# Kernel tuning notes

Hardware: AMD Instinct MI355X
Metric: run time of the kernel (lower is better)

## Reference

```python
import jax, jax.numpy as jnp
import numpy as np

# Config values (from c.mean_shift / c.cuda in the original module)
EMBED_DIM = 32      # embedding_dim
BW = 2.0            # kernel_bandwidth
ETA = 0.5           # step_size
N_ITERS = 3         # nb_iterations
RES = 96            # pic_res (image is RES x RES, N = RES*RES pixels)


def setup_inputs() -> dict:
    key = jax.random.key(0)
    # Scale 0.1 keeps exp(BW * x^T x) well inside fp32 range, mimicking the
    # bounded embeddings produced by the upstream margin-loss-trained net.
    x_in = 0.1 * jax.random.normal(key, (1, EMBED_DIM, RES, RES), dtype=jnp.float32)
    return {"x_in": x_in}


def reference(x_in):
    # x_in: (1, D, RES, RES). One mean-shift step per iteration:
    #   K = exp(bw * X^T X)                      (N x N affinity)
    #   deg_j = sum_i K[i, j]                    (column degree; K is symmetric)
    #   X_new = eta * X @ (K / deg) + (1-eta) * X
    # (The original's torch.inverse(diag(deg)) is exactly 1/deg column scaling.)
    # All iterates are concatenated along dim 0, as in the torch code.
    res = x_in.shape[3]
    n = res * res
    xs = [x_in.reshape(EMBED_DIM, n)]
    for _ in range(N_ITERS):
        X = xs[-1]                                    # (D, N)
        K = jnp.exp(BW * jnp.einsum('di,dj->ij', X, X))  # (N, N)
        deg = K.sum(axis=0)                           # (N,) column sums
        xs.append(ETA * (X @ (K / deg)) + (1.0 - ETA) * X)
    # (N_ITERS+1, D, RES, RES)
    return jnp.stack(xs, axis=0).reshape(-1, EMBED_DIM, res, res)
```

## Files before the change

kernel.cpp:

```cpp
#include <hip/hip_runtime.h>
#include <hip/hip_bf16.h>


#define DIM 32
#define RESO 96
#define NPT (RESO * RESO)
#define NITER 3
#define ETA 0.5f
#define SCALE 2.88539008f

#define QB 128
#define NQB (NPT / QB)
#define KSEG 7
#define NCHUNK128 (NPT / 128)

typedef __bf16 bf16_t;
typedef __bf16 v8bf __attribute__((ext_vector_type(8)));
typedef float  v4f  __attribute__((ext_vector_type(4)));

__device__ __forceinline__ void gload_lds16(const bf16_t* g, bf16_t* l) {
    __builtin_amdgcn_global_load_lds(
        (const __attribute__((address_space(1))) void*)g,
        (__attribute__((address_space(3))) void*)l, 16, 0, 0);
}

__device__ __forceinline__ int keyinv(int m) {
    return ((m & 8) << 1) | ((m & 4) << 1) | ((m & 16) >> 2) | (m & 3);
}

__global__ __launch_bounds__(256, 4)
void pack_kernel(const float* __restrict__ X,
                 bf16_t* __restrict__ rows,
                 bf16_t* __restrict__ cols,
                 float* __restrict__ out_copy) {
    __shared__ float tt[32][33];
    const int tid = threadIdx.x;
    const int n0  = blockIdx.x * 32;
    const int inv = keyinv(tid & 31);

#pragma unroll
    for (int j = 0; j < 4; ++j) {
        int d = (tid >> 5) + j * 8;
        int n = tid & 31;
        float v = X[(size_t)d * NPT + n0 + n];
        tt[d][n] = v;
        cols[(size_t)d * NPT + n0 + inv] = (bf16_t)v;
        out_copy[(size_t)d * NPT + n0 + n] = v;
    }
    __syncthreads();

#pragma unroll
    for (int j = 0; j < 4; ++j) {
        int n = (tid >> 5) + j * 8;
        int d = tid & 31;
        rows[(size_t)(n0 + n) * DIM + d] = (bf16_t)tt[d][n];
    }
}

__global__ __launch_bounds__(512, 4)
void msattn_kernel(const float* __restrict__ Xcur,
                   const bf16_t* __restrict__ rows,
                   const bf16_t* __restrict__ cols,
                   float* __restrict__ part_num,
                   float* __restrict__ part_den) {
    __shared__ __align__(16) bf16_t tiles[2][8192];

    const int tid  = threadIdx.x;
    const int w    = tid >> 6;
    const int lane = tid & 63;
    const int quad = lane >> 4;
    const int l16  = lane & 15;
    const int qb   = blockIdx.x;
    const int ks   = blockIdx.y;
    const int c0   = (NCHUNK128 * ks) / KSEG;
    const int c1   = (NCHUNK128 * (ks + 1)) / KSEG;
    const int q0w  = qb * QB + w * 16;

    v8bf qfrag;
#pragma unroll
    for (int j = 0; j < 8; ++j) {
        float v = Xcur[(quad * 8 + j) * NPT + q0w + l16];
        qfrag[j] = (bf16_t)(v * SCALE);
    }

    v8bf ones;
#pragma unroll
    for (int j = 0; j < 8; ++j) ones[j] = (bf16_t)1.0f;

    const bf16_t* gsrc;
    int gdelta, hdelta, dstoff;
    if (w < 4) {
        gsrc = rows + ((size_t)c0 * 128 + w * 16 + l16) * DIM + quad * 8;
        gdelta = 128 * DIM;
        hdelta = 64 * DIM;
        dstoff = w * 512;
    } else {
        int r = w - 4, hh = r >> 1, g = r & 1;
        gsrc = cols + (size_t)(hh * 16 + l16) * NPT + c0 * 128 + g * 32 + quad * 8;
        gdelta = 128;
        hdelta = 64;
        dstoff = 2048 + (w - 4) * 512;
    }

    v4f acc0 = {0.f, 0.f, 0.f, 0.f};
    v4f acc1 = {0.f, 0.f, 0.f, 0.f};
    v4f dden = {0.f, 0.f, 0.f, 0.f};

    gload_lds16(gsrc,          &tiles[0][dstoff]);
    gload_lds16(gsrc + hdelta, &tiles[0][4096 + dstoff]);
    gsrc += gdelta;
    __syncthreads();

    for (int c = c0; c < c1; ++c) {
        const int cc = c - c0;
        const bf16_t* tb = tiles[cc & 1];

        if (c + 1 < c1) {
            bf16_t* nt = tiles[(cc + 1) & 1];
            gload_lds16(gsrc,          &nt[dstoff]);
            gload_lds16(gsrc + hdelta, &nt[4096 + dstoff]);
            gsrc += gdelta;
        }

#pragma unroll
        for (int h = 0; h < 2; ++h) {
            const bf16_t* th = tb + h * 4096;

            v4f s[4];
#pragma unroll
            for (int t = 0; t < 4; ++t) {
                v8bf ka = *(const v8bf*)&th[t * 512 + lane * 8];
                s[t] = __builtin_amdgcn_mfma_f32_16x16x32_bf16(ka, qfrag,
                           (v4f){0.f, 0.f, 0.f, 0.f}, 0, 0, 0);
            }

            v8bf b00 = *(const v8bf*)&th[2048 + 0 * 512 + lane * 8];
            v8bf b01 = *(const v8bf*)&th[2048 + 1 * 512 + lane * 8];
            v8bf b10 = *(const v8bf*)&th[2048 + 2 * 512 + lane * 8];
            v8bf b11 = *(const v8bf*)&th[2048 + 3 * 512 + lane * 8];

            v8bf pa0, pa1;
#pragma unroll
            for (int t = 0; t < 2; ++t)
#pragma unroll
                for (int r = 0; r < 4; ++r)
                    pa0[t * 4 + r] = (bf16_t)__builtin_amdgcn_exp2f(s[t][r]);
#pragma unroll
            for (int t = 0; t < 2; ++t)
#pragma unroll
                for (int r = 0; r < 4; ++r)
                    pa1[t * 4 + r] = (bf16_t)__builtin_amdgcn_exp2f(s[2 + t][r]);

            acc0 = __builtin_amdgcn_mfma_f32_16x16x32_bf16(pa0, b00, acc0, 0, 0, 0);
            acc1 = __builtin_amdgcn_mfma_f32_16x16x32_bf16(pa0, b10, acc1, 0, 0, 0);
            dden = __builtin_amdgcn_mfma_f32_16x16x32_bf16(pa0, ones, dden, 0, 0, 0);
            acc0 = __builtin_amdgcn_mfma_f32_16x16x32_bf16(pa1, b01, acc0, 0, 0, 0);
            acc1 = __builtin_amdgcn_mfma_f32_16x16x32_bf16(pa1, b11, acc1, 0, 0, 0);
            dden = __builtin_amdgcn_mfma_f32_16x16x32_bf16(pa1, ones, dden, 0, 0, 0);
        }

        __syncthreads();
    }

    float* pn = part_num + (size_t)ks * NPT * DIM;
#pragma unroll
    for (int r = 0; r < 4; ++r) {
        int gq = q0w + quad * 4 + r;
        pn[(size_t)gq * DIM + l16]      = acc0[r];
        pn[(size_t)gq * DIM + 16 + l16] = acc1[r];
    }
    if (l16 == 0) {
#pragma unroll
        for (int r = 0; r < 4; ++r)
            part_den[ks * NPT + q0w + quad * 4 + r] = dden[r];
    }
}

__global__ __launch_bounds__(256, 4)
void reduce_kernel(const float* __restrict__ part_num,
                   const float* __restrict__ part_den,
                   const float* __restrict__ Xcur,
                   float* __restrict__ Xnext,
                   bf16_t* __restrict__ rows_out,
                   bf16_t* __restrict__ cols_out) {
    __shared__ float tnum[32][33];
    __shared__ float txn[32][33];
    __shared__ float tden[32];

    const int tid = threadIdx.x;
    const int q0  = blockIdx.x * 32;
    const int inv = keyinv(tid & 31);

    {
        int qq = tid >> 3, dq = tid & 7;
        v4f s = {0.f, 0.f, 0.f, 0.f};
#pragma unroll
        for (int ss = 0; ss < KSEG; ++ss)
            s += *(const v4f*)&part_num[((size_t)ss * NPT + q0 + qq) * DIM + dq * 4];
#pragma unroll
        for (int k = 0; k < 4; ++k) tnum[qq][dq * 4 + k] = s[k];
    }
    if (tid < 32) {
        float s = 0.f;
#pragma unroll
        for (int ss = 0; ss < KSEG; ++ss)
            s += part_den[ss * NPT + q0 + tid];
        tden[tid] = s;
    }
    __syncthreads();

#pragma unroll
    for (int j = 0; j < 4; ++j) {
        int idx = tid + j * 256;
        int d = idx >> 5, qq = idx & 31;
        float num = tnum[qq][d];
        float dn  = tden[qq];
        float xo  = Xcur[d * NPT + q0 + qq];
        float xn  = ETA * num / dn + (1.0f - ETA) * xo;
        Xnext[d * NPT + q0 + qq] = xn;
        cols_out[(size_t)d * NPT + q0 + inv] = (bf16_t)xn;
        txn[qq][d] = xn;
    }
    __syncthreads();

#pragma unroll
    for (int j = 0; j < 4; ++j) {
        int idx = tid + j * 256;
        int qq = idx >> 5, d = idx & 31;
        rows_out[(size_t)(q0 + qq) * DIM + d] = (bf16_t)txn[qq][d];
    }
}

extern "C" void kernel_launch(void* const* d_in, const int* in_sizes, int n_in,
                              void* d_out, int out_size, void* d_ws, size_t ws_size,
                              hipStream_t stream) {
    const float* x_in = (const float*)d_in[0];
    float* out = (float*)d_out;

    const size_t DN = (size_t)DIM * NPT;
    bf16_t* rows0 = (bf16_t*)d_ws;
    bf16_t* cols0 = rows0 + DN;
    bf16_t* rows1 = cols0 + DN;
    bf16_t* cols1 = rows1 + DN;
    float* part_num = (float*)(cols1 + DN);
    float* part_den = part_num + (size_t)KSEG * NPT * DIM;

    pack_kernel<<<NPT / 32, 256, 0, stream>>>(x_in, rows0, cols0, out);

    for (int it = 0; it < NITER; ++it) {
        const float* Xcur = (it == 0) ? x_in : out + (size_t)it * DN;
        bf16_t* rin  = (it & 1) ? rows1 : rows0;
        bf16_t* cin  = (it & 1) ? cols1 : cols0;
        bf16_t* rout = (it & 1) ? rows0 : rows1;
        bf16_t* cout = (it & 1) ? cols0 : cols1;
        msattn_kernel<<<dim3(NQB, KSEG), 512, 0, stream>>>(Xcur, rin, cin,
                                                           part_num, part_den);
        reduce_kernel<<<NPT / 32, 256, 0, stream>>>(part_num, part_den, Xcur,
                                                    out + (size_t)(it + 1) * DN,
                                                    rout, cout);
    }
}
```

Baseline: 125.5 us.

## Fuse split-K reduction into attention kernel via last-block atomic counter

Removes the separate reduce kernel. Each attention block now bumps a per-query-block atomic counter, and the last of the KSEG segment blocks to finish sums the partial numerators and denominators. That block then writes the next iterate plus its bf16 row and column copies. This cuts one kernel launch per iteration and its launch gap, at the cost of a serialized reduction tail on the last block and extra fences and atomics.

```diff
diff --git a/kernel.cpp b/kernel.cpp
--- a/kernel.cpp
+++ b/kernel.cpp
@@ -32,11 +32,14 @@
 void pack_kernel(const float* __restrict__ X,
                  bf16_t* __restrict__ rows,
                  bf16_t* __restrict__ cols,
-                 float* __restrict__ out_copy) {
+                 float* __restrict__ out_copy,
+                 int* __restrict__ counters) {
     __shared__ float tt[32][33];
     const int tid = threadIdx.x;
     const int n0  = blockIdx.x * 32;
     const int inv = keyinv(tid & 31);
+
+    if (blockIdx.x == 0 && tid < NQB) counters[tid] = 0;
 
 #pragma unroll
     for (int j = 0; j < 4; ++j) {
@@ -62,8 +65,13 @@
                    const bf16_t* __restrict__ rows,
                    const bf16_t* __restrict__ cols,
                    float* __restrict__ part_num,
-                   float* __restrict__ part_den) {
+                   float* __restrict__ part_den,
+                   float* __restrict__ Xnext,
+                   bf16_t* __restrict__ rows_out,
+                   bf16_t* __restrict__ cols_out,
+                   int* __restrict__ counters) {
     __shared__ __align__(16) bf16_t tiles[2][8192];
+    __shared__ int sflag;
 
     const int tid  = threadIdx.x;
     const int w    = tid >> 6;
@@ -174,60 +182,59 @@
         for (int r = 0; r < 4; ++r)
             part_den[ks * NPT + q0w + quad * 4 + r] = dden[r];
     }
-}
-
-__global__ __launch_bounds__(256, 4)
-void reduce_kernel(const float* __restrict__ part_num,
-                   const float* __restrict__ part_den,
-                   const float* __restrict__ Xcur,
-                   float* __restrict__ Xnext,
-                   bf16_t* __restrict__ rows_out,
-                   bf16_t* __restrict__ cols_out) {
-    __shared__ float tnum[32][33];
-    __shared__ float txn[32][33];
-    __shared__ float tden[32];
-
-    const int tid = threadIdx.x;
-    const int q0  = blockIdx.x * 32;
-    const int inv = keyinv(tid & 31);
-
-    {
-        int qq = tid >> 3, dq = tid & 7;
-        v4f s = {0.f, 0.f, 0.f, 0.f};
+
+    __syncthreads();
+    if (tid == 0) {
+        __threadfence();
+        sflag = __hip_atomic_fetch_add(&counters[qb], 1, __ATOMIC_ACQ_REL,
+                                       __HIP_MEMORY_SCOPE_AGENT);
+    }
+    __syncthreads();
+    if (sflag != KSEG - 1) return;
+    __threadfence();
+    if (tid == 0) counters[qb] = 0;
+
+    float* xsc = (float*)&tiles[0][0];
+    float* dsc = xsc + 128 * 33;
+    const int q0 = qb * QB;
+
+    if (tid < 128) {
+        float sd = 0.f;
+#pragma unroll
+        for (int ss = 0; ss < KSEG; ++ss) sd += part_den[ss * NPT + q0 + tid];
+        dsc[tid] = sd;
+    }
+    __syncthreads();
+
+#pragma unroll
+    for (int j = 0; j < 8; ++j) {
+        int e = j * 512 + tid;
+        int q = e >> 5, d = e & 31;
+        float sn = 0.f;
 #pragma unroll
         for (int ss = 0; ss < KSEG; ++ss)
-            s += *(const v4f*)&part_num[((size_t)ss * NPT + q0 + qq) * DIM + dq * 4];
-#pragma unroll
-        for (int k = 0; k < 4; ++k) tnum[qq][dq * 4 + k] = s[k];
-    }
-    if (tid < 32) {
-        float s = 0.f;
-#pragma unroll
-        for (int ss = 0; ss < KSEG; ++ss)
-            s += part_den[ss * NPT + q0 + tid];
-        tden[tid] = s;
-    }
-    __syncthreads();
-
-#pragma unroll
-    for (int j = 0; j < 4; ++j) {
-        int idx = tid + j * 256;
-        int d = idx >> 5, qq = idx & 31;
-        float num = tnum[qq][d];
-        float dn  = tden[qq];
-        float xo  = Xcur[d * NPT + q0 + qq];
-        float xn  = ETA * num / dn + (1.0f - ETA) * xo;
-        Xnext[d * NPT + q0 + qq] = xn;
-        cols_out[(size_t)d * NPT + q0 + inv] = (bf16_t)xn;
-        txn[qq][d] = xn;
-    }
-    __syncthreads();
-
-#pragma unroll
-    for (int j = 0; j < 4; ++j) {
-        int idx = tid + j * 256;
-        int qq = idx >> 5, d = idx & 31;
-        rows_out[(size_t)(q0 + qq) * DIM + d] = (bf16_t)txn[qq][d];
+            sn += part_num[((size_t)ss * NPT + q0 + q) * DIM + d];
+        xsc[q * 33 + d] = sn;
+    }
+    __syncthreads();
+
+#pragma unroll
+    for (int j = 0; j < 8; ++j) {
+        int e = j * 512 + tid;
+        int d = e >> 7, q = e & 127;
+        float xn = ETA * xsc[q * 33 + d] / dsc[q]
+                 + (1.0f - ETA) * Xcur[(size_t)d * NPT + q0 + q];
+        Xnext[(size_t)d * NPT + q0 + q] = xn;
+        cols_out[(size_t)d * NPT + q0 + (q & ~31) + keyinv(q & 31)] = (bf16_t)xn;
+        xsc[q * 33 + d] = xn;
+    }
+    __syncthreads();
+
+#pragma unroll
+    for (int j = 0; j < 8; ++j) {
+        int e = j * 512 + tid;
+        int q = e >> 5, d = e & 31;
+        rows_out[(size_t)(q0 + q) * DIM + d] = (bf16_t)xsc[q * 33 + d];
     }
 }
 
@@ -244,8 +251,9 @@
     bf16_t* cols1 = rows1 + DN;
     float* part_num = (float*)(cols1 + DN);
     float* part_den = part_num + (size_t)KSEG * NPT * DIM;
-
-    pack_kernel<<<NPT / 32, 256, 0, stream>>>(x_in, rows0, cols0, out);
+    int* counters   = (int*)(part_den + (size_t)KSEG * NPT);
+
+    pack_kernel<<<NPT / 32, 256, 0, stream>>>(x_in, rows0, cols0, out, counters);
 
     for (int it = 0; it < NITER; ++it) {
         const float* Xcur = (it == 0) ? x_in : out + (size_t)it * DN;
@@ -253,10 +261,8 @@
         bf16_t* cin  = (it & 1) ? cols1 : cols0;
         bf16_t* rout = (it & 1) ? rows0 : rows1;
         bf16_t* cout = (it & 1) ? cols0 : cols1;
-        msattn_kernel<<<dim3(NQB, KSEG), 512, 0, stream>>>(Xcur, rin, cin,
-                                                           part_num, part_den);
-        reduce_kernel<<<NPT / 32, 256, 0, stream>>>(part_num, part_den, Xcur,
-                                                    out + (size_t)(it + 1) * DN,
-                                                    rout, cout);
-    }
-}
+        msattn_kernel<<<dim3(NQB, KSEG), 512, 0, stream>>>(
+            Xcur, rin, cin, part_num, part_den,
+            out + (size_t)(it + 1) * DN, rout, cout, counters);
+    }
+}
```

New measurement: 221.0 us. +76.0%, slower.

## Process two query groups per wave to reuse loaded key tiles

Applied to the files above, without the earlier changes.

Each block now handles 256 queries instead of 128, and each wave keeps two query fragments and two sets of accumulators. Every key/value tile staged in LDS is therefore used for twice as many queries, halving global-to-LDS traffic and LDS reads per unit of work. The cost is higher register pressure (launch bounds lowered to 2 blocks per SM) and half as many blocks in the grid (36x7), which reduces the parallelism available across the device.

```diff
diff --git a/kernel.cpp b/kernel.cpp
--- a/kernel.cpp
+++ b/kernel.cpp
@@ -9,7 +9,7 @@
 #define ETA 0.5f
 #define SCALE 2.88539008f
 
-#define QB 128
+#define QB 256
 #define NQB (NPT / QB)
 #define KSEG 7
 #define NCHUNK128 (NPT / 128)
@@ -57,7 +57,7 @@
     }
 }
 
-__global__ __launch_bounds__(512, 4)
+__global__ __launch_bounds__(512, 2)
 void msattn_kernel(const float* __restrict__ Xcur,
                    const bf16_t* __restrict__ rows,
                    const bf16_t* __restrict__ cols,
@@ -76,11 +76,13 @@
     const int c1   = (NCHUNK128 * (ks + 1)) / KSEG;
     const int q0w  = qb * QB + w * 16;
 
-    v8bf qfrag;
+    v8bf qfrag0, qfrag1;
 #pragma unroll
     for (int j = 0; j < 8; ++j) {
-        float v = Xcur[(quad * 8 + j) * NPT + q0w + l16];
-        qfrag[j] = (bf16_t)(v * SCALE);
+        float v0 = Xcur[(quad * 8 + j) * NPT + q0w + l16];
+        float v1 = Xcur[(quad * 8 + j) * NPT + q0w + 128 + l16];
+        qfrag0[j] = (bf16_t)(v0 * SCALE);
+        qfrag1[j] = (bf16_t)(v1 * SCALE);
     }
 
     v8bf ones;
@@ -102,9 +104,12 @@
         dstoff = 2048 + (w - 4) * 512;
     }
 
-    v4f acc0 = {0.f, 0.f, 0.f, 0.f};
-    v4f acc1 = {0.f, 0.f, 0.f, 0.f};
-    v4f dden = {0.f, 0.f, 0.f, 0.f};
+    v4f acc00 = {0.f, 0.f, 0.f, 0.f};
+    v4f acc01 = {0.f, 0.f, 0.f, 0.f};
+    v4f acc10 = {0.f, 0.f, 0.f, 0.f};
+    v4f acc11 = {0.f, 0.f, 0.f, 0.f};
+    v4f dden0 = {0.f, 0.f, 0.f, 0.f};
+    v4f dden1 = {0.f, 0.f, 0.f, 0.f};
 
     gload_lds16(gsrc,          &tiles[0][dstoff]);
     gload_lds16(gsrc + hdelta, &tiles[0][4096 + dstoff]);
@@ -126,12 +131,14 @@
         for (int h = 0; h < 2; ++h) {
             const bf16_t* th = tb + h * 4096;
 
-            v4f s[4];
+            v4f sg0[4], sg1[4];
 #pragma unroll
             for (int t = 0; t < 4; ++t) {
                 v8bf ka = *(const v8bf*)&th[t * 512 + lane * 8];
-                s[t] = __builtin_amdgcn_mfma_f32_16x16x32_bf16(ka, qfrag,
-                           (v4f){0.f, 0.f, 0.f, 0.f}, 0, 0, 0);
+                sg0[t] = __builtin_amdgcn_mfma_f32_16x16x32_bf16(ka, qfrag0,
+                             (v4f){0.f, 0.f, 0.f, 0.f}, 0, 0, 0);
+                sg1[t] = __builtin_amdgcn_mfma_f32_16x16x32_bf16(ka, qfrag1,
+                             (v4f){0.f, 0.f, 0.f, 0.f}, 0, 0, 0);
             }
 
             v8bf b00 = *(const v8bf*)&th[2048 + 0 * 512 + lane * 8];
@@ -143,20 +150,30 @@
 #pragma unroll
             for (int t = 0; t < 2; ++t)
 #pragma unroll
-                for (int r = 0; r < 4; ++r)
-                    pa0[t * 4 + r] = (bf16_t)__builtin_amdgcn_exp2f(s[t][r]);
+                for (int r = 0; r < 4; ++r) {
+                    pa0[t * 4 + r] = (bf16_t)__builtin_amdgcn_exp2f(sg0[t][r]);
+                    pa1[t * 4 + r] = (bf16_t)__builtin_amdgcn_exp2f(sg0[2 + t][r]);
+                }
+            acc00 = __builtin_amdgcn_mfma_f32_16x16x32_bf16(pa0, b00, acc00, 0, 0, 0);
+            acc01 = __builtin_amdgcn_mfma_f32_16x16x32_bf16(pa0, b10, acc01, 0, 0, 0);
+            dden0 = __builtin_amdgcn_mfma_f32_16x16x32_bf16(pa0, ones, dden0, 0, 0, 0);
+            acc00 = __builtin_amdgcn_mfma_f32_16x16x32_bf16(pa1, b01, acc00, 0, 0, 0);
+            acc01 = __builtin_amdgcn_mfma_f32_16x16x32_bf16(pa1, b11, acc01, 0, 0, 0);
+            dden0 = __builtin_amdgcn_mfma_f32_16x16x32_bf16(pa1, ones, dden0, 0, 0, 0);
+
 #pragma unroll
             for (int t = 0; t < 2; ++t)
 #pragma unroll
-                for (int r = 0; r < 4; ++r)
-                    pa1[t * 4 + r] = (bf16_t)__builtin_amdgcn_exp2f(s[2 + t][r]);
-
-            acc0 = __builtin_amdgcn_mfma_f32_16x16x32_bf16(pa0, b00, acc0, 0, 0, 0);
-            acc1 = __builtin_amdgcn_mfma_f32_16x16x32_bf16(pa0, b10, acc1, 0, 0, 0);
-            dden = __builtin_amdgcn_mfma_f32_16x16x32_bf16(pa0, ones, dden, 0, 0, 0);
-            acc0 = __builtin_amdgcn_mfma_f32_16x16x32_bf16(pa1, b01, acc0, 0, 0, 0);
-            acc1 = __builtin_amdgcn_mfma_f32_16x16x32_bf16(pa1, b11, acc1, 0, 0, 0);
-            dden = __builtin_amdgcn_mfma_f32_16x16x32_bf16(pa1, ones, dden, 0, 0, 0);
+                for (int r = 0; r < 4; ++r) {
+                    pa0[t * 4 + r] = (bf16_t)__builtin_amdgcn_exp2f(sg1[t][r]);
+                    pa1[t * 4 + r] = (bf16_t)__builtin_amdgcn_exp2f(sg1[2 + t][r]);
+                }
+            acc10 = __builtin_amdgcn_mfma_f32_16x16x32_bf16(pa0, b00, acc10, 0, 0, 0);
+            acc11 = __builtin_amdgcn_mfma_f32_16x16x32_bf16(pa0, b10, acc11, 0, 0, 0);
+            dden1 = __builtin_amdgcn_mfma_f32_16x16x32_bf16(pa0, ones, dden1, 0, 0, 0);
+            acc10 = __builtin_amdgcn_mfma_f32_16x16x32_bf16(pa1, b01, acc10, 0, 0, 0);
+            acc11 = __builtin_amdgcn_mfma_f32_16x16x32_bf16(pa1, b11, acc11, 0, 0, 0);
+            dden1 = __builtin_amdgcn_mfma_f32_16x16x32_bf16(pa1, ones, dden1, 0, 0, 0);
         }
 
         __syncthreads();
@@ -165,14 +182,19 @@
     float* pn = part_num + (size_t)ks * NPT * DIM;
 #pragma unroll
     for (int r = 0; r < 4; ++r) {
-        int gq = q0w + quad * 4 + r;
-        pn[(size_t)gq * DIM + l16]      = acc0[r];
-        pn[(size_t)gq * DIM + 16 + l16] = acc1[r];
+        int gq0 = q0w + quad * 4 + r;
+        int gq1 = gq0 + 128;
+        pn[(size_t)gq0 * DIM + l16]      = acc00[r];
+        pn[(size_t)gq0 * DIM + 16 + l16] = acc01[r];
+        pn[(size_t)gq1 * DIM + l16]      = acc10[r];
+        pn[(size_t)gq1 * DIM + 16 + l16] = acc11[r];
     }
     if (l16 == 0) {
 #pragma unroll
-        for (int r = 0; r < 4; ++r)
-            part_den[ks * NPT + q0w + quad * 4 + r] = dden[r];
+        for (int r = 0; r < 4; ++r) {
+            part_den[ks * NPT + q0w + quad * 4 + r]       = dden0[r];
+            part_den[ks * NPT + q0w + 128 + quad * 4 + r] = dden1[r];
+        }
     }
 }
 
```

New measurement: 126.5 us. Within noise of the previous version (+0.8%).
